# Performance work log

Hardware: AMD Instinct MI355X
Metric: run time of the kernel (lower is better)

The kernel has to match this reference:

```python
import jax, jax.numpy as jnp
import numpy as np

C = 512; H = 64; W = 64; STRIDE = 16; NA = 9; IMG = 1024
PRE_NMS = 6000; POST_NMS = 300; NMS_T = 0.7; MIN_SIZE = 16.0
BBOX_CLIP = float(np.log(1000.0 / 16.0))  # standard dw/dh clamp for exp() safety


def _make_anchors():
    # 3 scales x 3 aspect ratios on a stride-16 grid -> (H*W*9, 4) xyxy anchors
    scales = np.array([128.0, 256.0, 512.0])
    ratios = np.array([0.5, 1.0, 2.0])
    hs = (scales[:, None] * np.sqrt(ratios)[None, :]).ravel()
    ws = (scales[:, None] / np.sqrt(ratios)[None, :]).ravel()
    yy, xx = np.meshgrid((np.arange(H) + 0.5) * STRIDE, (np.arange(W) + 0.5) * STRIDE, indexing='ij')
    ctr = np.stack([xx.ravel(), yy.ravel()], -1)            # (HW, 2) centers
    wh = np.stack([ws, hs], -1)                              # (9, 2)
    anc = np.concatenate([ctr[:, None, :] - 0.5 * wh[None], ctr[:, None, :] + 0.5 * wh[None]], -1)
    return anc.reshape(-1, 4).astype(np.float32)             # (HW*9, 4)


def setup_inputs() -> dict:
    key = jax.random.key(0)
    k = jax.random.split(key, 4)
    return {
        'feature_map': jax.random.normal(k[0], (1, C, H, W), jnp.float32),
        'anchors': jnp.asarray(_make_anchors()),
        'image_shape': jnp.array([IMG, IMG], jnp.int32),
        'conv1_w': 0.01 * jax.random.normal(k[1], (C, C, 3, 3), jnp.float32),
        'conv1_b': jnp.zeros((C,), jnp.float32),
        'cls_w': 0.01 * jax.random.normal(k[2], (NA, C, 1, 1), jnp.float32),
        'cls_b': jnp.zeros((NA,), jnp.float32),
        'box_w': 0.01 * jax.random.normal(k[3], (NA * 4, C, 1, 1), jnp.float32),
        'box_b': jnp.zeros((NA * 4,), jnp.float32),
    }


def _conv(x, w, b):
    dn = ('NCHW', 'OIHW', 'NCHW')
    return jax.lax.conv_general_dilated(x, w, (1, 1), 'SAME', dimension_numbers=dn) + b[None, :, None, None]


def _decode_boxes(deltas, anchors):
    aw = anchors[:, 2] - anchors[:, 0]
    ah = anchors[:, 3] - anchors[:, 1]
    ax = anchors[:, 0] + 0.5 * aw
    ay = anchors[:, 1] + 0.5 * ah
    dx, dy, dw, dh = deltas[:, 0], deltas[:, 1], deltas[:, 2], deltas[:, 3]
    dw = jnp.minimum(dw, BBOX_CLIP)
    dh = jnp.minimum(dh, BBOX_CLIP)
    px = dx * aw + ax
    py = dy * ah + ay
    pw = jnp.exp(dw) * aw
    ph = jnp.exp(dh) * ah
    return jnp.stack([px - 0.5 * pw, py - 0.5 * ph, px + 0.5 * pw, py + 0.5 * ph], -1)


def _pairwise_iou(a, b):
    area_a = (a[:, 2] - a[:, 0]) * (a[:, 3] - a[:, 1])
    area_b = (b[:, 2] - b[:, 0]) * (b[:, 3] - b[:, 1])
    lt = jnp.maximum(a[:, None, :2], b[None, :, :2])
    rb = jnp.minimum(a[:, None, 2:], b[None, :, 2:])
    wh = jnp.clip(rb - lt, 0.0)
    inter = wh[..., 0] * wh[..., 1]
    union = area_a[:, None] + area_b[None, :] - inter
    return jnp.where(union > 0, inter / union, 0.0)


def reference(feature_map, anchors, image_shape, conv1_w, conv1_b, cls_w, cls_b, box_w, box_b):
    # conv head
    y = jax.nn.relu(_conv(feature_map, conv1_w, conv1_b))
    scores = _conv(y, cls_w, cls_b).reshape(-1)            # (H*W*9,)  torch .view(-1) order
    deltas = _conv(y, box_w, box_b).reshape(-1, 4)         # (H*W*9, 4) torch .reshape(-1,4) order
    preds = _decode_boxes(deltas, anchors)

    # filter_proposals: sigmoid -> topk 6000 -> clamp -> min-size -> NMS(0.7) -> top 300
    s = jax.nn.sigmoid(scores)
    topv, topi = jax.lax.top_k(s, PRE_NMS)                  # sorted descending
    b = preds[topi]
    h_img = image_shape[0].astype(jnp.float32)
    w_img = image_shape[1].astype(jnp.float32)
    b = jnp.stack([jnp.clip(b[:, 0], 0.0, w_img), jnp.clip(b[:, 1], 0.0, h_img),
                   jnp.clip(b[:, 2], 0.0, w_img), jnp.clip(b[:, 3], 0.0, h_img)], -1)
    valid = ((b[:, 2] - b[:, 0]) >= MIN_SIZE) & ((b[:, 3] - b[:, 1]) >= MIN_SIZE)

    iou = _pairwise_iou(b, b)                               # (6000, 6000)
    idx = jnp.arange(PRE_NMS)

    def body(i, keep):  # greedy NMS in score order (boxes already sorted desc)
        sup = (iou[i] > NMS_T) & keep[i] & (idx > i)
        return keep & (~sup)

    keep = jax.lax.fori_loop(0, PRE_NMS, body, valid)
    fs = jnp.where(keep, topv, -1.0)                        # suppressed/invalid -> sentinel
    sc, i2 = jax.lax.top_k(fs, POST_NMS)
    return b[i2], sc
```

## Files before the change

kernel.cpp:

```cpp
#include <hip/hip_runtime.h>
#include <hip/hip_bf16.h>

typedef unsigned int u32;
typedef unsigned long long u64;
typedef float v2f __attribute__((ext_vector_type(2)));
typedef float v4f __attribute__((ext_vector_type(4)));

#define OFF_Y      0ull
#define OFF_WT     8388608ull
#define OFF_ZPART  8388608ull
#define OFF_SCORES 11337728ull
#define OFF_DRAW   11485184ull
#define OFF_HIST   12075008ull
#define OFF_TOPV   12665344ull
#define OFF_BOXES  12714496ull
#define OFF_VW     12812800ull
#define OFF_MASK   12813824ull

#define NS     36864
#define PRE    6000
#define POST   300
#define SORTN  8192
#define MROW   96

__global__ __launch_bounds__(256) void k_wtrans(const float* __restrict__ gw,
                                                float* __restrict__ wT) {
    int o = blockIdx.x * 256 + threadIdx.x;
    if (o >= 512 * 512 * 9) return;
    int ci = o / 4608;
    int r = o - ci * 4608;
    int k = r >> 9;
    int co = r & 511;
    wT[o] = gw[co * 4608 + ci * 9 + k];
}

#define CI 16
#define XROW 66
#define CHUNK_ELEMS (CI * 3 * XROW)
#define STAGE_IT 13
__global__ __launch_bounds__(256, 4) void k_conv1(const float* __restrict__ x,
                                                  const float* __restrict__ wT,
                                                  const float* __restrict__ gb,
                                                  float* __restrict__ y) {
    __shared__ float xs[CHUNK_ELEMS];
    const int t = threadIdx.x;
    const int tx = t & 63;
    const int wv = __builtin_amdgcn_readfirstlane(t >> 6);
    const int cob = (blockIdx.x & 15) << 5;
    const int h0 = blockIdx.x >> 4;
    const int co_base = cob + (wv << 3);

    int offs[STAGE_IT];
    u32 vmask = 0;
#pragma unroll
    for (int u = 0; u < STAGE_IT; ++u) {
        int idx = t + u * 256;
        offs[u] = 0;
        if (idx < CHUNK_ELEMS) {
            int ci = idx / (3 * XROW);
            int rem = idx - ci * (3 * XROW);
            int row = rem / XROW;
            int col = rem - row * XROW;
            int gr = h0 + row - 1, gc = col - 1;
            if ((unsigned)gr < 64u && (unsigned)gc < 64u) {
                offs[u] = ci * 4096 + (gr << 6) + gc;
                vmask |= 1u << u;
            }
        }
    }

    v2f acc2[4];
#pragma unroll
    for (int j = 0; j < 4; ++j) acc2[j] = (v2f){0.f, 0.f};

    float st[STAGE_IT];
#pragma unroll
    for (int u = 0; u < STAGE_IT; ++u)
        st[u] = (vmask >> u & 1) ? x[offs[u]] : 0.f;

#pragma unroll 1
    for (int cc = 0; cc < 32; ++cc) {
        if (cc) __syncthreads();
#pragma unroll
        for (int u = 0; u < STAGE_IT; ++u) {
            int idx = t + u * 256;
            if (idx < CHUNK_ELEMS) xs[idx] = st[u];
        }
        __syncthreads();
        if (cc + 1 < 32) {
            const float* xsrc = x + (cc + 1) * CI * 4096;
#pragma unroll
            for (int u = 0; u < STAGE_IT; ++u)
                st[u] = (vmask >> u & 1) ? xsrc[offs[u]] : 0.f;
        }

        const int cig0 = cc * CI;
#pragma unroll 2
        for (int ci = 0; ci < CI; ++ci) {
            float xr[9];
            {
                const float* xp = xs + ci * (3 * XROW) + tx;
#pragma unroll
                for (int r = 0; r < 3; ++r) {
                    xr[r * 3 + 0] = xp[r * XROW + 0];
                    xr[r * 3 + 1] = xp[r * XROW + 1];
                    xr[r * 3 + 2] = xp[r * XROW + 2];
                }
            }
            const float* wk = wT + (size_t)(cig0 + ci) * 4608 + co_base;
#pragma unroll
            for (int k = 0; k < 9; ++k) {
                v4f wa = *(const v4f*)(wk + k * 512);
                v4f wb = *(const v4f*)(wk + k * 512 + 4);
                float xv = xr[k];
                v2f xp2 = {xv, xv};
                acc2[0] = __builtin_elementwise_fma(__builtin_shufflevector(wa, wa, 0, 1), xp2, acc2[0]);
                acc2[1] = __builtin_elementwise_fma(__builtin_shufflevector(wa, wa, 2, 3), xp2, acc2[1]);
                acc2[2] = __builtin_elementwise_fma(__builtin_shufflevector(wb, wb, 0, 1), xp2, acc2[2]);
                acc2[3] = __builtin_elementwise_fma(__builtin_shufflevector(wb, wb, 2, 3), xp2, acc2[3]);
            }
        }
    }

#pragma unroll
    for (int j = 0; j < 4; ++j) {
        int co0 = co_base + 2 * j;
        float v0 = acc2[j].x + gb[co0];
        float v1 = acc2[j].y + gb[co0 + 1];
        v0 = v0 > 0.f ? v0 : 0.f;
        v1 = v1 > 0.f ? v1 : 0.f;
        y[co0 * 4096 + (h0 << 6) + tx] = v0;
        y[(co0 + 1) * 4096 + (h0 << 6) + tx] = v1;
    }
}

__global__ __launch_bounds__(256) void k_heads_part(const float* __restrict__ y,
                                                    const float* __restrict__ cw,
                                                    const float* __restrict__ bw,
                                                    float* __restrict__ zpart,
                                                    u32* __restrict__ hist) {
    __shared__ __align__(16) float ys[64][132];
    const int t = threadIdx.x;
    {
        int hb = blockIdx.x << 9;
        hist[hb + t] = 0u;
        hist[hb + 256 + t] = 0u;
    }
    const int px = t & 63;
    const int gu = __builtin_amdgcn_readfirstlane(t >> 6);
    const int px0 = (blockIdx.x & 63) << 6;
    const int q = blockIdx.x >> 6;
    const int cib = q << 7;
    const int nch = (gu == 0) ? 12 : 11;

    const float* wrow[12];
#pragma unroll
    for (int j = 0; j < 12; ++j) {
        int ch = gu + 4 * j;
        if (ch < 9) wrow[j] = cw + ch * 512;
        else if (ch < 45) wrow[j] = bw + (ch - 9) * 512;
        else wrow[j] = cw;
    }
    float acc[12];
#pragma unroll
    for (int j = 0; j < 12; ++j) acc[j] = 0.f;

    for (int idx = t; idx < 128 * 64; idx += 256) {
        int ci = idx >> 6;
        int pp = idx & 63;
        ys[pp][ci] = y[(cib + ci) * 4096 + px0 + pp];
    }
    __syncthreads();

#pragma unroll 1
    for (int cq = 0; cq < 32; ++cq) {
        float4 yv = *(const float4*)&ys[px][cq << 2];
        float4 wv[12];
#pragma unroll
        for (int j = 0; j < 12; ++j)
            if (j < nch) wv[j] = *(const float4*)(wrow[j] + cib + (cq << 2));
#pragma unroll
        for (int j = 0; j < 12; ++j)
            if (j < nch)
                acc[j] += wv[j].x * yv.x + wv[j].y * yv.y + wv[j].z * yv.z + wv[j].w * yv.w;
    }
    for (int j = 0; j < nch; ++j) {
        int ch = gu + 4 * j;
        zpart[((q * 45 + ch) << 12) + px0 + px] = acc[j];
    }
}

__global__ __launch_bounds__(256) void k_hreduce(const float* __restrict__ zpart,
                                                 const float* __restrict__ cb,
                                                 const float* __restrict__ bb,
                                                 float* __restrict__ scores,
                                                 float* __restrict__ draw,
                                                 u32* __restrict__ hist) {
    int i = blockIdx.x * 256 + threadIdx.x;
    if (i >= 45 * 4096) return;
    int ch = i >> 12;
    int sp = i & 4095;
    float z = zpart[((0 * 45 + ch) << 12) + sp] + zpart[((1 * 45 + ch) << 12) + sp] +
              zpart[((2 * 45 + ch) << 12) + sp] + zpart[((3 * 45 + ch) << 12) + sp];
    if (ch < 9) {
        z += cb[ch];
        float s = 1.f / (1.f + expf(-z));
        scores[(ch << 12) + sp] = s;
        u32 sb = __float_as_uint(s);
        atomicAdd(&hist[sb >> 13], 1u);
    } else {
        z += bb[ch - 9];
        draw[((ch - 9) << 12) + sp] = z;
    }
}

__global__ __launch_bounds__(1024) void k_select(const u32* __restrict__ hist,
                                                 const float* __restrict__ scores,
                                                 const float* __restrict__ draw,
                                                 const float* __restrict__ anchors,
                                                 const int* __restrict__ ishape,
                                                 float* __restrict__ boxes,
                                                 float* __restrict__ topv,
                                                 u64* __restrict__ vw) {
    __shared__ u32 csum[1024];
    __shared__ u32 suf[1024];
    __shared__ u64 sk[SORTN];
    __shared__ int sel_s, cnt_s;
    const int t = threadIdx.x;

    u32 s = 0;
    const u32* hp = hist + t * 128;
    for (int i = 0; i < 128; ++i) s += hp[i];
    csum[t] = s;
    suf[t] = s;
    if (t == 0) cnt_s = 0;
    __syncthreads();
    for (int off = 1; off < 1024; off <<= 1) {
        u32 v = suf[t] + ((t + off < 1024) ? suf[t + off] : 0u);
        __syncthreads();
        suf[t] = v;
        __syncthreads();
    }
    u32 above = suf[t] - csum[t];
    if (above < (u32)PRE && suf[t] >= (u32)PRE) {
        u32 run = above;
        int bstar = t * 128;
        u32 found = 0;
        for (int b2 = 127; b2 >= 0; --b2) {
            u32 c = hp[b2];
            if (!found && run + c >= (u32)PRE) { bstar = t * 128 + b2; found = 1; }
            if (!found) run += c;
        }
        sel_s = bstar;
    }
    for (int i = t; i < SORTN; i += 1024) sk[i] = 0;
    __syncthreads();

    const int sel = sel_s;
    for (int i = t; i < NS; i += 1024) {
        u32 sb = __float_as_uint(scores[i]);
        if ((int)(sb >> 13) >= sel) {
            int p = atomicAdd(&cnt_s, 1);
            if (p < SORTN) sk[p] = ((u64)sb << 32) | (u32)(~i);
        }
    }
    __syncthreads();

    const int base = t << 3;
    u64 a[8];
    {
#pragma unroll
        for (int u = 0; u < 8; ++u) a[u] = sk[base + u];
#pragma unroll
        for (int k = 2; k <= 8; k <<= 1) {
#pragma unroll
            for (int j = k >> 1; j > 0; j >>= 1) {
#pragma unroll
                for (int u = 0; u < 8; ++u) {
                    if ((u & j) == 0) {
                        int l = u | j;
                        bool up = (((base + u) & k) == 0);
                        u64 x0 = a[u], x1 = a[l];
                        if (up ? (x0 < x1) : (x0 > x1)) { a[u] = x1; a[l] = x0; }
                    }
                }
            }
        }
#pragma unroll
        for (int u = 0; u < 8; ++u) sk[base + u] = a[u];
        __syncthreads();
    }
    for (int k = 16; k <= SORTN; k <<= 1) {
        for (int j = k >> 1; j >= 8; j >>= 1) {
#pragma unroll
            for (int s2 = 0; s2 < 4; ++s2) {
                int pidx = t + (s2 << 10);
                int i = ((pidx & ~(j - 1)) << 1) | (pidx & (j - 1));
                int l = i | j;
                u64 x0 = sk[i], x1 = sk[l];
                bool up = ((i & k) == 0);
                if (up ? (x0 < x1) : (x0 > x1)) { sk[i] = x1; sk[l] = x0; }
            }
            __syncthreads();
        }
#pragma unroll
        for (int u = 0; u < 8; ++u) a[u] = sk[base + u];
        {
            bool up = ((base & k) == 0);
#pragma unroll
            for (int j = 4; j > 0; j >>= 1) {
#pragma unroll
                for (int u = 0; u < 8; ++u) {
                    if ((u & j) == 0) {
                        int l = u | j;
                        u64 x0 = a[u], x1 = a[l];
                        if (up ? (x0 < x1) : (x0 > x1)) { a[u] = x1; a[l] = x0; }
                    }
                }
            }
        }
#pragma unroll
        for (int u = 0; u < 8; ++u) sk[base + u] = a[u];
        __syncthreads();
    }

    const float wimg = (float)ishape[1], himg = (float)ishape[0];
#pragma unroll 1
    for (int s2 = 0; s2 < 6; ++s2) {
        int r = (s2 << 10) + t;
        bool valid = false;
        if (r < PRE) {
            u64 key = sk[r];
            u32 sb = (u32)(key >> 32);
            int i = (int)(~(u32)key);
            topv[r] = __uint_as_float(sb);
            int c = i >> 10;
            int t4 = i & 1023;
            float4 d4 = *(const float4*)(draw + c * 4096 + (t4 << 2));
            float4 a4 = *(const float4*)(anchors + i * 4);
            float aw = a4.z - a4.x, ah = a4.w - a4.y;
            float ax = a4.x + 0.5f * aw, ay = a4.y + 0.5f * ah;
            const float CLIPV = (float)4.135166556742356;
            float dw = fminf(d4.z, CLIPV);
            float dh = fminf(d4.w, CLIPV);
            float px = d4.x * aw + ax, py = d4.y * ah + ay;
            float pw = expf(dw) * aw, ph = expf(dh) * ah;
            float x1 = fminf(fmaxf(px - 0.5f * pw, 0.f), wimg);
            float y1 = fminf(fmaxf(py - 0.5f * ph, 0.f), himg);
            float x2 = fminf(fmaxf(px + 0.5f * pw, 0.f), wimg);
            float y2 = fminf(fmaxf(py + 0.5f * ph, 0.f), himg);
            valid = (x2 - x1 >= 16.f) && (y2 - y1 >= 16.f);
            *(float4*)(boxes + r * 4) = make_float4(x1, y1, x2, y2);
        }
        u64 bm = __ballot(valid);
        if ((t & 63) == 0) vw[(s2 << 4) + (t >> 6)] = bm;
    }
}

__global__ __launch_bounds__(256) void k_mask(const float* __restrict__ boxes,
                                              u64* __restrict__ mask) {
    __shared__ float4 cbx[16 * 65];
    const int t = threadIdx.x;
    const int r0 = blockIdx.x << 4;
    const int row = r0 + (t >> 4);
    const int wloc = t & 15;
    float4 rb = *(const float4*)(boxes + row * 4);
    float area_a = (rb.z - rb.x) * (rb.w - rb.y);
    for (int chunk = 0; chunk < 6; ++chunk) {
        int j0c = chunk << 10;
        for (int idx = t; idx < 1024; idx += 256) {
            int j = j0c + idx;
            float4 v = make_float4(0.f, 0.f, 0.f, 0.f);
            if (j < PRE) v = *(const float4*)(boxes + j * 4);
            cbx[(idx >> 6) * 65 + (idx & 63)] = v;
        }
        __syncthreads();
        u64 bits = 0;
        const float4* cbr = cbx + wloc * 65;
        for (int b = 0; b < 64; ++b) {
            int j = j0c + (wloc << 6) + b;
            float4 ob = cbr[b];
            float area_b = (ob.z - ob.x) * (ob.w - ob.y);
            float ltx = fmaxf(rb.x, ob.x), lty = fmaxf(rb.y, ob.y);
            float rbx = fminf(rb.z, ob.z), rby = fminf(rb.w, ob.w);
            float wx = fmaxf(rbx - ltx, 0.f), wy = fmaxf(rby - lty, 0.f);
            float inter = wx * wy;
            float uni = area_a + area_b - inter;
            float iou = (uni > 0.f) ? (inter / uni) : 0.f;
            if (iou > 0.7f && j > row && j < PRE) bits |= (1ull << b);
        }
        mask[(size_t)row * MROW + (chunk << 4) + wloc] = bits;
        __syncthreads();
    }
}

__global__ __launch_bounds__(320) void k_nms_out(const u64* __restrict__ mask,
                                                 const u64* __restrict__ vw,
                                                 const float* __restrict__ boxes,
                                                 const float* __restrict__ topv,
                                                 float* __restrict__ out) {
    __shared__ u64 rem[MROW];
    __shared__ u64 rows16[16][MROW];
    __shared__ u64 kws[MROW];
    __shared__ int keepl[POST];
    const int tid = threadIdx.x;
    for (int i = tid; i < MROW; i += 320) { rem[i] = 0ull; kws[i] = 0ull; }
    __syncthreads();
    int kc = 0;
    bool done = false;
    for (int w = 0; w < 94 && !done; ++w) {
        u64 aw = vw[w] & ~rem[w];
        u64 kwbits = 0;
        while (aw != 0ull && !done) {
            int bq[16];
            u64 tmp = aw;
#pragma unroll
            for (int q2 = 0; q2 < 16; ++q2) {
                bq[q2] = tmp ? __builtin_ctzll(tmp) : 64;
                tmp &= tmp - 1;
            }
#pragma unroll
            for (int u = 0; u < 5; ++u) {
                int i = tid + u * 320;
                if (i < 16 * MROW) {
                    int q2 = i / MROW;
                    int ww = i - q2 * MROW;
                    if (bq[q2] < 64)
                        rows16[q2][ww] = mask[(size_t)((w << 6) + bq[q2]) * MROW + ww];
                }
            }
            __syncthreads();
            for (int q2 = 0; q2 < 16; ++q2) {
                int b = bq[q2];
                if (b >= 64) break;
                if (!((aw >> b) & 1ull)) continue;
                if (tid == 0) keepl[kc] = (w << 6) + b;
                kc++;
                kwbits |= (1ull << b);
                if (kc >= POST) { done = true; break; }
                if (tid < MROW) rem[tid] |= rows16[q2][tid];
                aw &= ~rows16[q2][w];
                aw &= ~(1ull << b);
            }
            __syncthreads();
        }
        if (tid == 0) kws[w] = kwbits;
        __syncthreads();
    }
    __syncthreads();

    int j = tid;
    if (j >= POST) return;
    int kc2 = kc;
    int r;
    float sc;
    if (j < kc2) {
        r = keepl[j];
        sc = topv[r];
    } else {
        int target = j - kc2;
        r = PRE - 1;
        int cum = 0;
        for (int w = 0; w < 94; ++w) {
            u64 kb = kws[w];
            int nvalid = (w < 93) ? 64 : 48;
            u64 vmask2 = (nvalid == 64) ? ~0ull : ((1ull << nvalid) - 1ull);
            u64 nk = (~kb) & vmask2;
            int c = __popcll(nk);
            if (cum + c > target) {
                int need = target - cum;
                u64 m = nk;
                for (int q = 0; q < need; ++q) m &= (m - 1);
                r = (w << 6) + __builtin_ctzll(m);
                break;
            }
            cum += c;
        }
        sc = -1.0f;
    }
    out[j * 4 + 0] = boxes[r * 4 + 0];
    out[j * 4 + 1] = boxes[r * 4 + 1];
    out[j * 4 + 2] = boxes[r * 4 + 2];
    out[j * 4 + 3] = boxes[r * 4 + 3];
    out[1200 + j] = sc;
}

extern "C" void kernel_launch(void* const* d_in, const int* in_sizes, int n_in,
                              void* d_out, int out_size, void* d_ws, size_t ws_size,
                              hipStream_t stream) {
    const float* x = (const float*)d_in[0];
    const float* anchors = (const float*)d_in[1];
    const int* ishape = (const int*)d_in[2];
    const float* c1w = (const float*)d_in[3];
    const float* c1b = (const float*)d_in[4];
    const float* clw = (const float*)d_in[5];
    const float* clb = (const float*)d_in[6];
    const float* bxw = (const float*)d_in[7];
    const float* bxb = (const float*)d_in[8];

    char* ws = (char*)d_ws;
    float* y      = (float*)(ws + OFF_Y);
    float* wT     = (float*)(ws + OFF_WT);
    float* zpart  = (float*)(ws + OFF_ZPART);
    float* scores = (float*)(ws + OFF_SCORES);
    float* draw   = (float*)(ws + OFF_DRAW);
    u32*   hist   = (u32*)(ws + OFF_HIST);
    float* topv   = (float*)(ws + OFF_TOPV);
    float* boxes  = (float*)(ws + OFF_BOXES);
    u64*   vw     = (u64*)(ws + OFF_VW);
    u64*   mask   = (u64*)(ws + OFF_MASK);

    k_wtrans<<<(512 * 512 * 9 + 255) / 256, 256, 0, stream>>>(c1w, wT);
    k_conv1<<<1024, 256, 0, stream>>>(x, wT, c1b, y);
    k_heads_part<<<256, 256, 0, stream>>>(y, clw, bxw, zpart, hist);
    k_hreduce<<<(45 * 4096 + 255) / 256, 256, 0, stream>>>(zpart, clb, bxb, scores, draw, hist);
    k_select<<<1, 1024, 0, stream>>>(hist, scores, draw, anchors, ishape, boxes, topv, vw);
    k_mask<<<PRE / 16, 256, 0, stream>>>(boxes, mask);
    k_nms_out<<<1, 320, 0, stream>>>(mask, vw, boxes, topv, (float*)d_out);
}
```

Before: 712.9 us.

## Fuse 1x1 head partial sums and reduction into one kernel

The heads kernel no longer splits the 512 input channels into four partial blocks. Each block now loops over all four channel quarters and applies bias, sigmoid, the histogram atomic and the draw store directly, which removes the zpart buffer and the separate reduce kernel. Histogram clearing moves to a hipMemsetAsync, and the workspace layout is compacted. The cost is only 64 blocks instead of 256, so the heads stage has less parallelism on a large GPU.

Result: slower. 754.5 us (+5.8%).

```diff
diff --git a/kernel.cpp b/kernel.cpp
--- a/kernel.cpp
+++ b/kernel.cpp
@@ -8,20 +8,20 @@
 
 #define OFF_Y      0ull
 #define OFF_WT     8388608ull
-#define OFF_ZPART  8388608ull
-#define OFF_SCORES 11337728ull
-#define OFF_DRAW   11485184ull
-#define OFF_HIST   12075008ull
-#define OFF_TOPV   12665344ull
-#define OFF_BOXES  12714496ull
-#define OFF_VW     12812800ull
-#define OFF_MASK   12813824ull
+#define OFF_SCORES 8388608ull
+#define OFF_DRAW   8536064ull
+#define OFF_TOPV   9125888ull
+#define OFF_BOXES  9150464ull
+#define OFF_VW     9248768ull
+#define OFF_HIST   9249792ull
+#define OFF_MASK   9774080ull
 
 #define NS     36864
 #define PRE    6000
 #define POST   300
 #define SORTN  8192
 #define MROW   96
+#define HBINS  131072
 
 __global__ __launch_bounds__(256) void k_wtrans(const float* __restrict__ gw,
                                                 float* __restrict__ wT) {
@@ -134,23 +134,19 @@
     }
 }
 
-__global__ __launch_bounds__(256) void k_heads_part(const float* __restrict__ y,
-                                                    const float* __restrict__ cw,
-                                                    const float* __restrict__ bw,
-                                                    float* __restrict__ zpart,
-                                                    u32* __restrict__ hist) {
+__global__ __launch_bounds__(256) void k_heads(const float* __restrict__ y,
+                                               const float* __restrict__ cw,
+                                               const float* __restrict__ cb,
+                                               const float* __restrict__ bw,
+                                               const float* __restrict__ bb,
+                                               float* __restrict__ scores,
+                                               float* __restrict__ draw,
+                                               u32* __restrict__ hist) {
     __shared__ __align__(16) float ys[64][132];
     const int t = threadIdx.x;
-    {
-        int hb = blockIdx.x << 9;
-        hist[hb + t] = 0u;
-        hist[hb + 256 + t] = 0u;
-    }
     const int px = t & 63;
     const int gu = __builtin_amdgcn_readfirstlane(t >> 6);
-    const int px0 = (blockIdx.x & 63) << 6;
-    const int q = blockIdx.x >> 6;
-    const int cib = q << 7;
+    const int px0 = blockIdx.x << 6;
     const int nch = (gu == 0) ? 12 : 11;
 
     const float* wrow[12];
@@ -165,52 +161,41 @@
 #pragma unroll
     for (int j = 0; j < 12; ++j) acc[j] = 0.f;
 
-    for (int idx = t; idx < 128 * 64; idx += 256) {
-        int ci = idx >> 6;
-        int pp = idx & 63;
-        ys[pp][ci] = y[(cib + ci) * 4096 + px0 + pp];
-    }
-    __syncthreads();
-
 #pragma unroll 1
-    for (int cq = 0; cq < 32; ++cq) {
-        float4 yv = *(const float4*)&ys[px][cq << 2];
-        float4 wv[12];
-#pragma unroll
-        for (int j = 0; j < 12; ++j)
-            if (j < nch) wv[j] = *(const float4*)(wrow[j] + cib + (cq << 2));
-#pragma unroll
-        for (int j = 0; j < 12; ++j)
-            if (j < nch)
-                acc[j] += wv[j].x * yv.x + wv[j].y * yv.y + wv[j].z * yv.z + wv[j].w * yv.w;
+    for (int q = 0; q < 4; ++q) {
+        const int cib = q << 7;
+        if (q) __syncthreads();
+        for (int idx = t; idx < 128 * 64; idx += 256) {
+            int ci = idx >> 6;
+            int pp = idx & 63;
+            ys[pp][ci] = y[(cib + ci) * 4096 + px0 + pp];
+        }
+        __syncthreads();
+#pragma unroll 1
+        for (int cq = 0; cq < 32; ++cq) {
+            float4 yv = *(const float4*)&ys[px][cq << 2];
+            float4 wv[12];
+#pragma unroll
+            for (int j = 0; j < 12; ++j)
+                if (j < nch) wv[j] = *(const float4*)(wrow[j] + cib + (cq << 2));
+#pragma unroll
+            for (int j = 0; j < 12; ++j)
+                if (j < nch)
+                    acc[j] += wv[j].x * yv.x + wv[j].y * yv.y + wv[j].z * yv.z + wv[j].w * yv.w;
+        }
     }
     for (int j = 0; j < nch; ++j) {
         int ch = gu + 4 * j;
-        zpart[((q * 45 + ch) << 12) + px0 + px] = acc[j];
-    }
-}
-
-__global__ __launch_bounds__(256) void k_hreduce(const float* __restrict__ zpart,
-                                                 const float* __restrict__ cb,
-                                                 const float* __restrict__ bb,
-                                                 float* __restrict__ scores,
-                                                 float* __restrict__ draw,
-                                                 u32* __restrict__ hist) {
-    int i = blockIdx.x * 256 + threadIdx.x;
-    if (i >= 45 * 4096) return;
-    int ch = i >> 12;
-    int sp = i & 4095;
-    float z = zpart[((0 * 45 + ch) << 12) + sp] + zpart[((1 * 45 + ch) << 12) + sp] +
-              zpart[((2 * 45 + ch) << 12) + sp] + zpart[((3 * 45 + ch) << 12) + sp];
-    if (ch < 9) {
-        z += cb[ch];
-        float s = 1.f / (1.f + expf(-z));
-        scores[(ch << 12) + sp] = s;
-        u32 sb = __float_as_uint(s);
-        atomicAdd(&hist[sb >> 13], 1u);
-    } else {
-        z += bb[ch - 9];
-        draw[((ch - 9) << 12) + sp] = z;
+        int sp = px0 + px;
+        if (ch < 9) {
+            float z = acc[j] + cb[ch];
+            float s = 1.f / (1.f + expf(-z));
+            scores[(ch << 12) + sp] = s;
+            u32 sb = __float_as_uint(s);
+            atomicAdd(&hist[sb >> 13], 1u);
+        } else {
+            draw[((ch - 9) << 12) + sp] = acc[j] + bb[ch - 9];
+        }
     }
 }
 
@@ -451,14 +436,13 @@
 
     int j = tid;
     if (j >= POST) return;
-    int kc2 = kc;
     int r;
     float sc;
-    if (j < kc2) {
+    if (j < kc) {
         r = keepl[j];
         sc = topv[r];
     } else {
-        int target = j - kc2;
+        int target = j - kc;
         r = PRE - 1;
         int cum = 0;
         for (int w = 0; w < 94; ++w) {
@@ -501,7 +485,6 @@
     char* ws = (char*)d_ws;
     float* y      = (float*)(ws + OFF_Y);
     float* wT     = (float*)(ws + OFF_WT);
-    float* zpart  = (float*)(ws + OFF_ZPART);
     float* scores = (float*)(ws + OFF_SCORES);
     float* draw   = (float*)(ws + OFF_DRAW);
     u32*   hist   = (u32*)(ws + OFF_HIST);
@@ -512,8 +495,8 @@
 
     k_wtrans<<<(512 * 512 * 9 + 255) / 256, 256, 0, stream>>>(c1w, wT);
     k_conv1<<<1024, 256, 0, stream>>>(x, wT, c1b, y);
-    k_heads_part<<<256, 256, 0, stream>>>(y, clw, bxw, zpart, hist);
-    k_hreduce<<<(45 * 4096 + 255) / 256, 256, 0, stream>>>(zpart, clb, bxb, scores, draw, hist);
+    (void)hipMemsetAsync(hist, 0, HBINS * sizeof(u32), stream);
+    k_heads<<<64, 256, 0, stream>>>(y, clw, clb, bxw, bxb, scores, draw, hist);
     k_select<<<1, 1024, 0, stream>>>(hist, scores, draw, anchors, ishape, boxes, topv, vw);
     k_mask<<<PRE / 16, 256, 0, stream>>>(boxes, mask);
     k_nms_out<<<1, 320, 0, stream>>>(mask, vw, boxes, topv, (float*)d_out);
```
